# Kernel optimization log

Measured on AMD Instinct MI355X. Metric: run time of the kernel, lower is better.

The kernel has to match this reference:

```python
import jax, jax.numpy as jnp
import numpy as np

HEADS = 16
DIM_HEAD = 64
SCALE = DIM_HEAD ** -0.5


def setup_inputs() -> dict:
    key = jax.random.key(0)
    k1, k2, k3, k4 = jax.random.split(key, 4)
    dim = 1024
    inner = HEADS * DIM_HEAD  # 1024
    b, n = 4, 2048
    x = jax.random.normal(k1, (b, n, dim), dtype=jnp.float32)
    # weights stored as [in, out] (equivalent math to torch Linear)
    w_qkv = jax.random.normal(k2, (dim, inner * 3), dtype=jnp.float32) * (dim ** -0.5)
    w_out = jax.random.normal(k3, (inner, dim), dtype=jnp.float32) * (inner ** -0.5)
    b_out = jax.random.normal(k4, (dim,), dtype=jnp.float32) * 0.01
    return {"x": x, "w_qkv": w_qkv, "w_out": w_out, "b_out": b_out}


def reference(x, w_qkv, w_out, b_out):
    b, n, dim = x.shape
    qkv = x @ w_qkv                                   # [b, n, 3*inner]
    q, k, v = jnp.split(qkv, 3, axis=-1)
    def to_heads(t):
        return t.reshape(b, n, HEADS, DIM_HEAD).transpose(0, 2, 1, 3)  # b h n d
    q, k, v = to_heads(q) * SCALE, to_heads(k), to_heads(v)
    dots = jnp.einsum('bhid,bhjd->bhij', q, k)        # [b, h, n, n]
    mask_value = -jnp.finfo(dots.dtype).max
    causal_mask = jnp.triu(jnp.ones((n, n), dtype=bool), k=1)
    dots = jnp.where(causal_mask, mask_value, dots)
    attn = jax.nn.softmax(dots, axis=-1)
    out = jnp.einsum('bhij,bhjd->bhid', attn, v)      # [b, h, n, d]
    out = out.transpose(0, 2, 1, 3).reshape(b, n, HEADS * DIM_HEAD)
    return out @ w_out + b_out
```

## Files before the change

### kernel.cpp

```cpp
#include <hip/hip_runtime.h>
#include <hip/hip_bf16.h>
#include <stdint.h>

typedef __attribute__((ext_vector_type(8))) short bf16x8;
typedef __attribute__((ext_vector_type(4))) float f32x4;
typedef __attribute__((ext_vector_type(4))) unsigned int uint32x4;

#define TOKENS 8192
#define DMODEL 1024
#define NQKV   3072
#define NSEQ   2048
#define NHEAD  16
#define DHEAD  64

__device__ __forceinline__ ushort f32_bf16(float f) {
    uint32_t u = __builtin_bit_cast(uint32_t, f);
    u = (u + 0x7fffu + ((u >> 16) & 1u)) >> 16;
    return (ushort)u;
}

__device__ __forceinline__ unsigned int cvt_pk_bf16(float lo, float hi) {
    unsigned int r;
    asm("v_cvt_pk_bf16_f32 %0, %1, %2" : "=v"(r) : "v"(lo), "v"(hi));
    return r;
}
__device__ __forceinline__ void permlane32_swap(unsigned int& a, unsigned int& b) {
    asm("v_permlane32_swap_b32 %0, %1" : "+v"(a), "+v"(b));
}
__device__ __forceinline__ void permlane16_swap(unsigned int& a, unsigned int& b) {
    asm("v_permlane16_swap_b32 %0, %1" : "+v"(a), "+v"(b));
}
__device__ __forceinline__ unsigned opaque_copy(unsigned x) {
    unsigned y;
    asm("v_mov_b32 %0, %1" : "=v"(y) : "v"(x));
    return y;
}

__device__ __forceinline__ float red_max_g(float x) {
    unsigned a = __builtin_bit_cast(unsigned, x);
    unsigned b = opaque_copy(a);
    permlane16_swap(a, b);
    float r = fmaxf(__builtin_bit_cast(float, a), __builtin_bit_cast(float, b));
    unsigned c = __builtin_bit_cast(unsigned, r);
    unsigned d = opaque_copy(c);
    permlane32_swap(c, d);
    return fmaxf(__builtin_bit_cast(float, c), __builtin_bit_cast(float, d));
}
__device__ __forceinline__ float red_sum_g(float x) {
    unsigned a = __builtin_bit_cast(unsigned, x);
    unsigned b = opaque_copy(a);
    permlane16_swap(a, b);
    float r = __builtin_bit_cast(float, a) + __builtin_bit_cast(float, b);
    unsigned c = __builtin_bit_cast(unsigned, r);
    unsigned d = opaque_copy(c);
    permlane32_swap(c, d);
    return __builtin_bit_cast(float, c) + __builtin_bit_cast(float, d);
}

__device__ __forceinline__ void gload16(const void* g, void* l) {
    __builtin_amdgcn_global_load_lds(
        (const __attribute__((address_space(1))) void*)g,
        (__attribute__((address_space(3))) void*)l, 16, 0, 0);
}

__global__ void cvt_x_kernel(const float* __restrict__ x, ushort* __restrict__ xb) {
    int i = blockIdx.x * 256 + threadIdx.x;
    float4 v = reinterpret_cast<const float4*>(x)[i];
    ushort4 o;
    o.x = f32_bf16(v.x); o.y = f32_bf16(v.y);
    o.z = f32_bf16(v.z); o.w = f32_bf16(v.w);
    reinterpret_cast<ushort4*>(xb)[i] = o;
}

__global__ __launch_bounds__(256) void cvt_wt_kernel(
    const float* __restrict__ w, ushort* __restrict__ wt, int N)
{
    __shared__ float tile[64][65];
    const int tid = threadIdx.x;
    const int r  = tid >> 4;
    const int c4 = (tid & 15) * 4;
    const int n0 = blockIdx.x * 64;
    const int k0 = blockIdx.y * 64;
    #pragma unroll
    for (int i = 0; i < 4; ++i) {
        const float4 v = *reinterpret_cast<const float4*>(&w[(size_t)(k0 + r + i * 16) * N + n0 + c4]);
        tile[r + i * 16][c4 + 0] = v.x;
        tile[r + i * 16][c4 + 1] = v.y;
        tile[r + i * 16][c4 + 2] = v.z;
        tile[r + i * 16][c4 + 3] = v.w;
    }
    __syncthreads();
    #pragma unroll
    for (int i = 0; i < 4; ++i) {
        ushort4 o;
        o.x = f32_bf16(tile[c4 + 0][r + i * 16]);
        o.y = f32_bf16(tile[c4 + 1][r + i * 16]);
        o.z = f32_bf16(tile[c4 + 2][r + i * 16]);
        o.w = f32_bf16(tile[c4 + 3][r + i * 16]);
        *reinterpret_cast<ushort4*>(&wt[(size_t)(n0 + r + i * 16) * 1024 + k0 + c4]) = o;
    }
}

template<int MODE>
__global__ __launch_bounds__(256) void gemm_bt(
    const ushort* __restrict__ A, const ushort* __restrict__ Bt,
    ushort* __restrict__ Qb, ushort* __restrict__ Kb, ushort* __restrict__ Vtb,
    float* __restrict__ Out, const float* __restrict__ bias)
{
    constexpr int K = 1024;
    __shared__ __align__(16) ushort As[128 * 32];
    __shared__ __align__(16) ushort Bs[128 * 32];

    const int lane = threadIdx.x & 63;
    const int w    = threadIdx.x >> 6;
    const int l16  = lane & 15;
    const int g    = lane >> 4;
    const int row0 = blockIdx.y * 128;
    const int col0 = blockIdx.x * 128;
    const int wr   = (w >> 1) * 64;
    const int wc   = (w & 1) * 64;

    const int srow = w * 16 + (lane >> 2);
    const int scol = (lane & 3) * 8;
    const ushort* Ag = A  + (size_t)(row0 + srow) * K + scol;
    const ushort* Bg = Bt + (size_t)(col0 + srow) * K + scol;
    ushort* AsW = As + w * (16 * 32);
    ushort* BsW = Bs + w * (16 * 32);

    f32x4 acc[4][4] = {};

    for (int kk = 0; kk < K; kk += 32) {
        gload16(Ag + kk,          AsW);
        gload16(Ag + 64 * K + kk, AsW + 64 * 32);
        gload16(Bg + kk,          BsW);
        gload16(Bg + 64 * K + kk, BsW + 64 * 32);
        __syncthreads();
        bf16x8 a[4], b[4];
        #pragma unroll
        for (int m = 0; m < 4; ++m)
            a[m] = *reinterpret_cast<const bf16x8*>(&As[(wr + m * 16 + l16) * 32 + 8 * g]);
        #pragma unroll
        for (int n = 0; n < 4; ++n)
            b[n] = *reinterpret_cast<const bf16x8*>(&Bs[(wc + n * 16 + l16) * 32 + 8 * g]);
        #pragma unroll
        for (int m = 0; m < 4; ++m)
            #pragma unroll
            for (int n = 0; n < 4; ++n)
                acc[m][n] = __builtin_amdgcn_mfma_f32_16x16x32_bf16(a[m], b[n], acc[m][n], 0, 0, 0);
        __syncthreads();
    }

    if (MODE == 0) {
        const int part = col0 >> 10;
        const float QSC = 0.18033688011112042f;
        #pragma unroll
        for (int m = 0; m < 4; ++m) {
            const int trow = row0 + wr + m * 16 + 4 * g;
            #pragma unroll
            for (int n = 0; n < 4; ++n) {
                const int c  = col0 + wc + n * 16 + l16;
                const int cc = c & 1023;
                const int h  = cc >> 6, d = cc & 63;
                #pragma unroll
                for (int jj = 0; jj < 4; ++jj) {
                    const int t  = trow + jj;
                    const int bb = t >> 11, nn = t & 2047;
                    const float v = acc[m][n][jj];
                    const size_t bhid = (size_t)(bb * NHEAD + h);
                    if (part == 0)
                        Qb[(bhid * NSEQ + nn) * DHEAD + d] = f32_bf16(v * QSC);
                    else if (part == 1)
                        Kb[(bhid * NSEQ + nn) * DHEAD + d] = f32_bf16(v);
                    else
                        Vtb[bhid * (NSEQ * DHEAD) + (size_t)(nn >> 5) * (DHEAD * 32)
                            + d * 32 + (nn & 31)] = f32_bf16(v);
                }
            }
        }
    } else {
        #pragma unroll
        for (int m = 0; m < 4; ++m) {
            const int trow = row0 + wr + m * 16 + 4 * g;
            #pragma unroll
            for (int n = 0; n < 4; ++n) {
                const int c = col0 + wc + n * 16 + l16;
                const float bv = bias[c];
                #pragma unroll
                for (int jj = 0; jj < 4; ++jj)
                    Out[(size_t)(trow + jj) * DMODEL + c] = acc[m][n][jj] + bv;
            }
        }
    }
}

__device__ __forceinline__ void attn_qk(
    int kt, int qr0s, int l16, int g,
    const bf16x8 (&kk)[4][2],
    const bf16x8 qf0, const bf16x8 qf1,
    f32x4 (&oacc)[4], float& mrun, float& lsum,
    bf16x8& pf0, bf16x8& pf1)
{
    const f32x4 zero = {};
    f32x4 s[4];
    #pragma unroll
    for (int t = 0; t < 4; ++t) {
        s[t] = __builtin_amdgcn_mfma_f32_16x16x32_bf16(kk[t][0], qf0, zero, 0, 0, 0);
        s[t] = __builtin_amdgcn_mfma_f32_16x16x32_bf16(kk[t][1], qf1, s[t], 0, 0, 0);
    }
    if (kt + 63 > qr0s) {
        const int kb = kt + 4 * g - (qr0s + l16);
        #pragma unroll
        for (int t = 0; t < 4; ++t)
            #pragma unroll
            for (int jj = 0; jj < 4; ++jj)
                if (kb + 16 * t + jj > 0) s[t][jj] = -1e30f;
    }
    const float m0 = fmaxf(fmaxf(s[0][0], s[0][1]), s[0][2]);
    const float m1 = fmaxf(fmaxf(s[0][3], s[1][0]), s[1][1]);
    const float m2 = fmaxf(fmaxf(s[1][2], s[1][3]), s[2][0]);
    const float m3 = fmaxf(fmaxf(s[2][1], s[2][2]), s[2][3]);
    const float m4 = fmaxf(fmaxf(s[3][0], s[3][1]), s[3][2]);
    const float m5 = fmaxf(fmaxf(m0, m1), m2);
    const float m6 = fmaxf(fmaxf(m3, m4), s[3][3]);
    float mx = red_max_g(fmaxf(m5, m6));
    if (__any(mx > mrun + 8.0f)) {
        const float mn = fmaxf(mrun, mx);
        const float sc = __builtin_amdgcn_exp2f(mrun - mn);
        mrun = mn;
        lsum *= sc;
        float scj[4];
        #pragma unroll
        for (int jj = 0; jj < 4; ++jj) scj[jj] = __shfl(sc, 4 * g + jj);
        #pragma unroll
        for (int dt = 0; dt < 4; ++dt)
            #pragma unroll
            for (int jj = 0; jj < 4; ++jj) oacc[dt][jj] *= scj[jj];
    }
    float ps = 0.f;
    unsigned int pw[4][2];
    #pragma unroll
    for (int t = 0; t < 4; ++t) {
        const float p0 = __builtin_amdgcn_exp2f(s[t][0] - mrun);
        const float p1 = __builtin_amdgcn_exp2f(s[t][1] - mrun);
        const float p2 = __builtin_amdgcn_exp2f(s[t][2] - mrun);
        const float p3 = __builtin_amdgcn_exp2f(s[t][3] - mrun);
        ps += (p0 + p1) + (p2 + p3);
        pw[t][0] = cvt_pk_bf16(p0, p1);
        pw[t][1] = cvt_pk_bf16(p2, p3);
    }
    lsum += red_sum_g(ps);
    unsigned int a0 = pw[0][0], a1 = pw[0][1], b0 = pw[1][0], b1 = pw[1][1];
    permlane32_swap(a0, b0); permlane32_swap(a1, b1);
    permlane16_swap(a0, b0); permlane16_swap(a1, b1);
    pf0 = __builtin_bit_cast(bf16x8, (uint32x4){a0, a1, b0, b1});
    unsigned int c0 = pw[2][0], c1 = pw[2][1], d0 = pw[3][0], d1 = pw[3][1];
    permlane32_swap(c0, d0); permlane32_swap(c1, d1);
    permlane16_swap(c0, d0); permlane16_swap(c1, d1);
    pf1 = __builtin_bit_cast(bf16x8, (uint32x4){c0, c1, d0, d1});
}

__global__ __launch_bounds__(256) void attn_kernel(
    const ushort* __restrict__ Qb, const ushort* __restrict__ Kb,
    const ushort* __restrict__ Vt, ushort* __restrict__ Ob)
{
    __shared__ __align__(16) ushort Klds[2][4096];
    __shared__ __align__(16) ushort Vlds[2][4096];

    const int lane = threadIdx.x & 63;
    const int w    = threadIdx.x >> 6;
    const int l16  = lane & 15;
    const int g    = lane >> 4;

    const int bid = blockIdx.x;
    const int xcd = bid & 7, ii = bid >> 3;
    const int bh  = xcd * 8 + (ii >> 4);
    const int jlo = ii & 15;
    const int jhi = 31 - jlo;

    const int qr0_lo = jlo * 64 + w * 16;
    const int qr0_hi = jhi * 64 + w * 16;
    const int nt = jhi + 1;

    const ushort* QpL = Qb + ((size_t)bh * NSEQ + qr0_lo + l16) * DHEAD + 8 * g;
    const ushort* QpH = Qb + ((size_t)bh * NSEQ + qr0_hi + l16) * DHEAD + 8 * g;
    const bf16x8 qfL0 = *reinterpret_cast<const bf16x8*>(QpL);
    const bf16x8 qfL1 = *reinterpret_cast<const bf16x8*>(QpL + 32);
    const bf16x8 qfH0 = *reinterpret_cast<const bf16x8*>(QpH);
    const bf16x8 qfH1 = *reinterpret_cast<const bf16x8*>(QpH + 32);

    const ushort* Kg = Kb + (size_t)bh * (NSEQ * DHEAD);
    const ushort* Vg = Vt + (size_t)bh * (NSEQ * DHEAD);

    const int q0   = w * 2;
    const int kcol0 = (lane & 3) * 8;

    f32x4 oaccL[4] = {}, oaccH[4] = {};
    float mrunL = -1e30f, lsumL = 0.f, mrunH = -1e30f, lsumH = 0.f;

    {
        #pragma unroll
        for (int i = 0; i < 2; ++i) {
            const int q = q0 + i;
            const int h = q >> 2;
            gload16(Kg + (size_t)((q & 3) * 16 + (lane >> 2)) * 64 + h * 32 + kcol0,
                    &Klds[0][q * 512]);
            gload16(Vg + (size_t)q * 512 + lane * 8,
                    &Vlds[0][q * 512]);
        }
    }
    __syncthreads();

    for (int t = 0; t < nt; ++t) {
        const int cur = t & 1;
        if (t + 1 < nt) {
            const int kt1 = (t + 1) * 64;
            #pragma unroll
            for (int i = 0; i < 2; ++i) {
                const int q = q0 + i;
                const int h = q >> 2;
                gload16(Kg + (size_t)(kt1 + ((q & 3) * 16 + (lane >> 2))) * 64 + h * 32 + kcol0,
                        &Klds[cur ^ 1][q * 512]);
                gload16(Vg + (size_t)kt1 * 64 + q * 512 + lane * 8,
                        &Vlds[cur ^ 1][q * 512]);
            }
        }
        const int kt = t * 64;
        bf16x8 kk[4][2];
        #pragma unroll
        for (int tt = 0; tt < 4; ++tt) {
            #pragma unroll
            for (int h = 0; h < 2; ++h)
                kk[tt][h] = *reinterpret_cast<const bf16x8*>(
                    &Klds[cur][h * 2048 + (16 * tt + l16) * 32 + 8 * g]);
        }
        bf16x8 pfH0, pfH1, pfL0, pfL1;
        attn_qk(kt, qr0_hi, l16, g, kk, qfH0, qfH1, oaccH, mrunH, lsumH, pfH0, pfH1);
        const bool doLo = (t <= jlo);
        if (doLo)
            attn_qk(kt, qr0_lo, l16, g, kk, qfL0, qfL1, oaccL, mrunL, lsumL, pfL0, pfL1);
        #pragma unroll
        for (int dt = 0; dt < 4; ++dt) {
            const bf16x8 v0 = *reinterpret_cast<const bf16x8*>(
                &Vlds[cur][(dt * 16 + l16) * 32 + 8 * g]);
            const bf16x8 v1 = *reinterpret_cast<const bf16x8*>(
                &Vlds[cur][2048 + (dt * 16 + l16) * 32 + 8 * g]);
            oaccH[dt] = __builtin_amdgcn_mfma_f32_16x16x32_bf16(pfH0, v0, oaccH[dt], 0, 0, 0);
            oaccH[dt] = __builtin_amdgcn_mfma_f32_16x16x32_bf16(pfH1, v1, oaccH[dt], 0, 0, 0);
            if (doLo) {
                oaccL[dt] = __builtin_amdgcn_mfma_f32_16x16x32_bf16(pfL0, v0, oaccL[dt], 0, 0, 0);
                oaccL[dt] = __builtin_amdgcn_mfma_f32_16x16x32_bf16(pfL1, v1, oaccL[dt], 0, 0, 0);
            }
        }
        __syncthreads();
    }

    const int bb = bh >> 4, h = bh & 15;
    {
        const float inv = 1.0f / lsumH;
        float invj[4];
        #pragma unroll
        for (int jj = 0; jj < 4; ++jj) invj[jj] = __shfl(inv, 4 * g + jj);
        #pragma unroll
        for (int jj = 0; jj < 4; ++jj) {
            const size_t t = (size_t)bb * NSEQ + qr0_hi + 4 * g + jj;
            #pragma unroll
            for (int dt = 0; dt < 4; ++dt)
                Ob[t * DMODEL + h * DHEAD + dt * 16 + l16] = f32_bf16(oaccH[dt][jj] * invj[jj]);
        }
    }
    {
        const float inv = 1.0f / lsumL;
        float invj[4];
        #pragma unroll
        for (int jj = 0; jj < 4; ++jj) invj[jj] = __shfl(inv, 4 * g + jj);
        #pragma unroll
        for (int jj = 0; jj < 4; ++jj) {
            const size_t t = (size_t)bb * NSEQ + qr0_lo + 4 * g + jj;
            #pragma unroll
            for (int dt = 0; dt < 4; ++dt)
                Ob[t * DMODEL + h * DHEAD + dt * 16 + l16] = f32_bf16(oaccL[dt][jj] * invj[jj]);
        }
    }
}

extern "C" void kernel_launch(void* const* d_in, const int* in_sizes, int n_in,
                              void* d_out, int out_size, void* d_ws, size_t ws_size,
                              hipStream_t stream)
{
    const float* x     = (const float*)d_in[0];
    const float* w_qkv = (const float*)d_in[1];
    const float* w_out = (const float*)d_in[2];
    const float* b_out = (const float*)d_in[3];
    float* out = (float*)d_out;

    char* ws = (char*)d_ws;
    ushort* x_bf   = (ushort*)(ws);
    ushort* wqkv_t = (ushort*)(ws + 16777216);
    ushort* wout_t = (ushort*)(ws + 23068672);
    ushort* q_bf   = (ushort*)(ws + 25165824);
    ushort* k_bf   = (ushort*)(ws + 41943040);
    ushort* vt_bf  = (ushort*)(ws + 58720256);
    ushort* attn_bf = x_bf;

    cvt_x_kernel<<<dim3(TOKENS * DMODEL / 4 / 256), dim3(256), 0, stream>>>(x, x_bf);
    cvt_wt_kernel<<<dim3(NQKV / 64, 1024 / 64), dim3(256), 0, stream>>>(w_qkv, wqkv_t, NQKV);
    cvt_wt_kernel<<<dim3(1024 / 64, 1024 / 64), dim3(256), 0, stream>>>(w_out, wout_t, 1024);

    gemm_bt<0><<<dim3(NQKV / 128, TOKENS / 128), dim3(256), 0, stream>>>(
        x_bf, wqkv_t, q_bf, k_bf, vt_bf, nullptr, nullptr);

    attn_kernel<<<dim3(1024), dim3(256), 0, stream>>>(q_bf, k_bf, vt_bf, attn_bf);

    gemm_bt<1><<<dim3(DMODEL / 128, TOKENS / 128), dim3(256), 0, stream>>>(
        attn_bf, wout_t, nullptr, nullptr, nullptr, out, b_out);
}
```

Measured before the change: 215.9 us.

## XOR-swizzle LDS tiles in GEMM and attention, raise wave priority around MFMAs

The GEMM A/B tiles and the attention K/V tiles are now stored in LDS with an XOR swizzle on the 8-element column chunk. The global-load source columns and the fragment-read columns are permuted to match, which is meant to remove LDS bank conflicts on the 16-byte fragment reads. The V tile global-load addressing is remapped so it fits the same swizzled [row][32] layout. s_setprio is also raised around the QK and PV MFMA blocks to favour waves that are issuing matrix work. The risk is an addressing mismatch, and the priority hints may do little or may reorder scheduling badly.

Result: no change. 214.9 us (-0.5%).

```diff
diff --git a/kernel.cpp b/kernel.cpp
--- a/kernel.cpp
+++ b/kernel.cpp
@@ -12,6 +12,7 @@
 #define NSEQ   2048
 #define NHEAD  16
 #define DHEAD  64
+
 
 __device__ __forceinline__ ushort f32_bf16(float f) {
     uint32_t u = __builtin_bit_cast(uint32_t, f);
@@ -120,12 +121,14 @@
     const int wr   = (w >> 1) * 64;
     const int wc   = (w & 1) * 64;
 
-    const int srow = w * 16 + (lane >> 2);
-    const int scol = (lane & 3) * 8;
-    const ushort* Ag = A  + (size_t)(row0 + srow) * K + scol;
-    const ushort* Bg = Bt + (size_t)(col0 + srow) * K + scol;
+    const int srow  = w * 16 + (lane >> 2);
+    const int sswz8 = ((lane & 3) ^ ((lane >> 3) & 3)) * 8;
+    const ushort* Ag = A  + (size_t)(row0 + srow) * K + sswz8;
+    const ushort* Bg = Bt + (size_t)(col0 + srow) * K + sswz8;
     ushort* AsW = As + w * (16 * 32);
     ushort* BsW = Bs + w * (16 * 32);
+
+    const int cq8 = (g ^ ((l16 >> 1) & 3)) * 8;
 
     f32x4 acc[4][4] = {};
 
@@ -138,10 +141,10 @@
         bf16x8 a[4], b[4];
         #pragma unroll
         for (int m = 0; m < 4; ++m)
-            a[m] = *reinterpret_cast<const bf16x8*>(&As[(wr + m * 16 + l16) * 32 + 8 * g]);
+            a[m] = *reinterpret_cast<const bf16x8*>(&As[(wr + m * 16 + l16) * 32 + cq8]);
         #pragma unroll
         for (int n = 0; n < 4; ++n)
-            b[n] = *reinterpret_cast<const bf16x8*>(&Bs[(wc + n * 16 + l16) * 32 + 8 * g]);
+            b[n] = *reinterpret_cast<const bf16x8*>(&Bs[(wc + n * 16 + l16) * 32 + cq8]);
         #pragma unroll
         for (int m = 0; m < 4; ++m)
             #pragma unroll
@@ -202,11 +205,13 @@
 {
     const f32x4 zero = {};
     f32x4 s[4];
+    __builtin_amdgcn_s_setprio(1);
     #pragma unroll
     for (int t = 0; t < 4; ++t) {
         s[t] = __builtin_amdgcn_mfma_f32_16x16x32_bf16(kk[t][0], qf0, zero, 0, 0, 0);
         s[t] = __builtin_amdgcn_mfma_f32_16x16x32_bf16(kk[t][1], qf1, s[t], 0, 0, 0);
     }
+    __builtin_amdgcn_s_setprio(0);
     if (kt + 63 > qr0s) {
         const int kb = kt + 4 * g - (qr0s + l16);
         #pragma unroll
@@ -291,22 +296,21 @@
     const ushort* Kg = Kb + (size_t)bh * (NSEQ * DHEAD);
     const ushort* Vg = Vt + (size_t)bh * (NSEQ * DHEAD);
 
-    const int q0   = w * 2;
-    const int kcol0 = (lane & 3) * 8;
+    const int q0    = w * 2;
+    const int srow  = lane >> 2;
+    const int sswz8 = ((lane & 3) ^ ((lane >> 3) & 3)) * 8;
+    const int cq8   = (g ^ ((l16 >> 1) & 3)) * 8;
 
     f32x4 oaccL[4] = {}, oaccH[4] = {};
     float mrunL = -1e30f, lsumL = 0.f, mrunH = -1e30f, lsumH = 0.f;
 
-    {
-        #pragma unroll
-        for (int i = 0; i < 2; ++i) {
-            const int q = q0 + i;
-            const int h = q >> 2;
-            gload16(Kg + (size_t)((q & 3) * 16 + (lane >> 2)) * 64 + h * 32 + kcol0,
-                    &Klds[0][q * 512]);
-            gload16(Vg + (size_t)q * 512 + lane * 8,
-                    &Vlds[0][q * 512]);
-        }
+    #pragma unroll
+    for (int i = 0; i < 2; ++i) {
+        const int q = q0 + i;
+        gload16(Kg + (size_t)((q & 3) * 16 + srow) * 64 + (q >> 2) * 32 + sswz8,
+                &Klds[0][q * 512]);
+        gload16(Vg + (size_t)(q >> 2) * 2048 + ((q & 3) * 16 + srow) * 32 + sswz8,
+                &Vlds[0][q * 512]);
     }
     __syncthreads();
 
@@ -317,10 +321,9 @@
             #pragma unroll
             for (int i = 0; i < 2; ++i) {
                 const int q = q0 + i;
-                const int h = q >> 2;
-                gload16(Kg + (size_t)(kt1 + ((q & 3) * 16 + (lane >> 2))) * 64 + h * 32 + kcol0,
+                gload16(Kg + (size_t)(kt1 + (q & 3) * 16 + srow) * 64 + (q >> 2) * 32 + sswz8,
                         &Klds[cur ^ 1][q * 512]);
-                gload16(Vg + (size_t)kt1 * 64 + q * 512 + lane * 8,
+                gload16(Vg + (size_t)kt1 * 64 + (q >> 2) * 2048 + ((q & 3) * 16 + srow) * 32 + sswz8,
                         &Vlds[cur ^ 1][q * 512]);
             }
         }
@@ -331,19 +334,20 @@
             #pragma unroll
             for (int h = 0; h < 2; ++h)
                 kk[tt][h] = *reinterpret_cast<const bf16x8*>(
-                    &Klds[cur][h * 2048 + (16 * tt + l16) * 32 + 8 * g]);
+                    &Klds[cur][h * 2048 + (16 * tt + l16) * 32 + cq8]);
         }
         bf16x8 pfH0, pfH1, pfL0, pfL1;
         attn_qk(kt, qr0_hi, l16, g, kk, qfH0, qfH1, oaccH, mrunH, lsumH, pfH0, pfH1);
         const bool doLo = (t <= jlo);
         if (doLo)
             attn_qk(kt, qr0_lo, l16, g, kk, qfL0, qfL1, oaccL, mrunL, lsumL, pfL0, pfL1);
+        __builtin_amdgcn_s_setprio(1);
         #pragma unroll
         for (int dt = 0; dt < 4; ++dt) {
             const bf16x8 v0 = *reinterpret_cast<const bf16x8*>(
-                &Vlds[cur][(dt * 16 + l16) * 32 + 8 * g]);
+                &Vlds[cur][(dt * 16 + l16) * 32 + cq8]);
             const bf16x8 v1 = *reinterpret_cast<const bf16x8*>(
-                &Vlds[cur][2048 + (dt * 16 + l16) * 32 + 8 * g]);
+                &Vlds[cur][2048 + (dt * 16 + l16) * 32 + cq8]);
             oaccH[dt] = __builtin_amdgcn_mfma_f32_16x16x32_bf16(pfH0, v0, oaccH[dt], 0, 0, 0);
             oaccH[dt] = __builtin_amdgcn_mfma_f32_16x16x32_bf16(pfH1, v1, oaccH[dt], 0, 0, 0);
             if (doLo) {
@@ -351,6 +355,7 @@
                 oaccL[dt] = __builtin_amdgcn_mfma_f32_16x16x32_bf16(pfL1, v1, oaccL[dt], 0, 0, 0);
             }
         }
+        __builtin_amdgcn_s_setprio(0);
         __syncthreads();
     }
 
```
